# Optimization experiments

Hardware: AMD Instinct MI355X
Metric: run time of the kernel (lower is better)

The kernel has to match this reference:

```python
import jax, jax.numpy as jnp
import numpy as np

B, NM, D, H = 16384, 5, 256, 8
LN_EPS = 1e-5


def _ln(x, g, b):
    m = jnp.mean(x, axis=-1, keepdims=True)
    v = jnp.var(x, axis=-1, keepdims=True)
    return (x - m) / jnp.sqrt(v + LN_EPS) * g + b


def _mha(q_in, kv_in, Wi, bi, Wo, bo):
    # q_in: [B,1,D], kv_in: [B,1,D]; Wi: [3D,D] packed q/k/v like nn.MultiheadAttention
    Bq, Lq, Dm = q_in.shape
    Lk = kv_in.shape[1]
    dh = Dm // H
    q = (q_in @ Wi[:Dm].T + bi[:Dm]).reshape(Bq, Lq, H, dh).transpose(0, 2, 1, 3)
    k = (kv_in @ Wi[Dm:2 * Dm].T + bi[Dm:2 * Dm]).reshape(Bq, Lk, H, dh).transpose(0, 2, 1, 3)
    v = (kv_in @ Wi[2 * Dm:].T + bi[2 * Dm:]).reshape(Bq, Lk, H, dh).transpose(0, 2, 1, 3)
    scores = jnp.einsum('bhqd,bhkd->bhqk', q, k) * (1.0 / np.sqrt(dh))
    attn = jax.nn.softmax(scores, axis=-1)  # trivially 1.0 for Lk=1, kept for fidelity
    out = jnp.einsum('bhqk,bhkd->bhqd', attn, v).transpose(0, 2, 1, 3).reshape(Bq, Lq, Dm)
    return out @ Wo.T + bo


def setup_inputs() -> dict:
    key = jax.random.key(0)
    ks = jax.random.split(key, 8)
    s = 0.02
    return {
        'x': jax.random.normal(ks[0], (B, NM, D), jnp.float32),
        'self_Wi': jax.random.normal(ks[1], (3 * D, D), jnp.float32) * s,
        'self_bi': jnp.zeros((3 * D,), jnp.float32),
        'self_Wo': jax.random.normal(ks[2], (D, D), jnp.float32) * s,
        'self_bo': jnp.zeros((D,), jnp.float32),
        'cross_Wi': jax.random.normal(ks[3], (4, 3 * D, D), jnp.float32) * s,
        'cross_bi': jnp.zeros((4, 3 * D), jnp.float32),
        'cross_Wo': jax.random.normal(ks[4], (4, D, D), jnp.float32) * s,
        'cross_bo': jnp.zeros((4, D), jnp.float32),
        'cross_ln_g': jnp.ones((4, D), jnp.float32),
        'cross_ln_b': jnp.zeros((4, D), jnp.float32),
        'gate_ln_g': jnp.ones((D,), jnp.float32),
        'gate_ln_b': jnp.zeros((D,), jnp.float32),
        'gate_W': jax.random.normal(ks[5], (NM, D), jnp.float32) * s,
        'gate_b': jnp.zeros((NM,), jnp.float32),
        'final_ln_g': jnp.ones((D,), jnp.float32),
        'final_ln_b': jnp.zeros((D,), jnp.float32),
        'modal_idx': 2,
    }


def reference(x, self_Wi, self_bi, self_Wo, self_bo,
              cross_Wi, cross_bi, cross_Wo, cross_bo, cross_ln_g, cross_ln_b,
              gate_ln_g, gate_ln_b, gate_W, gate_b, final_ln_g, final_ln_b,
              modal_idx):
    query = x[:, modal_idx:modal_idx + 1, :]  # [B,1,D]
    self_out = _mha(query, query, self_Wi, self_bi, self_Wo, self_bo)

    other_idx = [i for i in range(NM) if i != modal_idx]
    kv = jnp.swapaxes(x[:, other_idx, :], 0, 1)[:, :, None, :]  # [4,B,1,D]

    def branch(Wi, bi, Wo, bo, g, b, kv_i):
        a = _mha(query, kv_i, Wi, bi, Wo, bo)
        return _ln(query + a, g, b)  # dropout is identity in eval

    cross_outs = jax.vmap(branch)(cross_Wi, cross_bi, cross_Wo, cross_bo,
                                  cross_ln_g, cross_ln_b, kv)  # [4,B,1,D]

    gates = jax.nn.softmax(_ln(query, gate_ln_g, gate_ln_b) @ gate_W.T + gate_b, axis=-1)  # [B,1,5]
    combined = gates[..., 0:1] * self_out + jnp.einsum('nbld,bln->bld', cross_outs, gates[..., 1:])
    return _ln(query + combined, final_ln_g, final_ln_b)
```

## Files before the change

kernel.cpp:

```cpp
#include <hip/hip_runtime.h>


typedef __attribute__((ext_vector_type(8))) short short8;
typedef __attribute__((ext_vector_type(4))) float floatx4;

__device__ __forceinline__ float b2f(unsigned short h) {
    union { unsigned int u; float f; } v; v.u = ((unsigned int)h) << 16; return v.f;
}
__device__ __forceinline__ unsigned short f2b(float f) {
    union { unsigned int u; float f; } v; v.f = f;
    unsigned int u = v.u;
    return (unsigned short)((u + 0x7FFFu + ((u >> 16) & 1u)) >> 16);
}

__global__ __launch_bounds__(256) void k_fuse(
    const float* __restrict__ sWi, const float* __restrict__ sbi,
    const float* __restrict__ sWo, const float* __restrict__ sbo,
    const float* __restrict__ cWi, const float* __restrict__ cbi,
    const float* __restrict__ cWo, const float* __restrict__ cbo,
    unsigned short* __restrict__ WF, float* __restrict__ BF)
{
    int s = blockIdx.y;
    int i0 = blockIdx.x * 4;
    int tid = threadIdx.x;
    const float *Wo, *Wv, *bv, *bo;
    if (s == 0) { Wo = sWo; Wv = sWi + 512 * 256; bv = sbi + 512; bo = sbo; }
    else {
        int n = s - 1;
        Wo = cWo + n * 65536;
        Wv = cWi + n * 768 * 256 + 512 * 256;
        bv = cbi + n * 768 + 512;
        bo = cbo + n * 256;
    }
    __shared__ float wo[4 * 256];
    #pragma unroll
    for (int it = 0; it < 4; ++it) {
        int idx = tid + it * 256;
        wo[idx] = Wo[i0 * 256 + idx];
    }
    __syncthreads();
    float a0 = 0.f, a1 = 0.f, a2 = 0.f, a3 = 0.f;
    for (int k = 0; k < 256; ++k) {
        float wv = Wv[k * 256 + tid];
        a0 += wo[k] * wv;
        a1 += wo[256 + k] * wv;
        a2 += wo[512 + k] * wv;
        a3 += wo[768 + k] * wv;
    }
    unsigned short* dst = WF + ((size_t)s * 256 + i0) * 256 + tid;
    dst[0] = f2b(a0); dst[256] = f2b(a1); dst[512] = f2b(a2); dst[768] = f2b(a3);
    if (tid < 4) {
        int i = i0 + tid;
        float bacc = 0.f;
        for (int k = 0; k < 256; ++k) bacc += Wo[i * 256 + k] * bv[k];
        BF[s * 256 + i] = bacc + bo[i];
    }
}

__device__ __forceinline__ float wred(float v) {
    #pragma unroll
    for (int o = 32; o > 0; o >>= 1) v += __shfl_xor(v, o, 64);
    return v;
}

__global__ __launch_bounds__(256) void k_main(
    const float* __restrict__ x, const unsigned short* __restrict__ WF,
    const float* __restrict__ BF,
    const float* __restrict__ cln_g, const float* __restrict__ cln_b,
    const float* __restrict__ gln_g, const float* __restrict__ gln_b,
    const float* __restrict__ gW, const float* __restrict__ gb,
    const float* __restrict__ fln_g, const float* __restrict__ fln_b,
    const int* __restrict__ midx, float* __restrict__ out)
{
    __shared__ __align__(16) unsigned short A[32 * 264];
    __shared__ __align__(16) unsigned short Yb[32 * 264];
    __shared__ float gWs[5 * 256];
    __shared__ float gLDS[32 * 8];

    int m = midx[0];
    int b0 = blockIdx.x * 32;
    int tid = threadIdx.x;
    int wave = tid >> 6, lane = tid & 63;
    int l16 = lane & 15, q4 = lane >> 4;
    int j = lane * 4;

    #pragma unroll
    for (int i = 0; i < 5; ++i) gWs[tid + i * 256] = gW[tid + i * 256];

    float qv[8][4];
    #pragma unroll
    for (int rr = 0; rr < 8; ++rr) {
        int r = wave * 8 + rr;
        float4 u = *(const float4*)(x + ((size_t)(b0 + r) * 5 + m) * 256 + j);
        qv[rr][0] = u.x; qv[rr][1] = u.y; qv[rr][2] = u.z; qv[rr][3] = u.w;
    }
    float4 glg = *(const float4*)(gln_g + j);
    float4 glb = *(const float4*)(gln_b + j);
    float gbv[5];
    #pragma unroll
    for (int n = 0; n < 5; ++n) gbv[n] = gb[n];

    __syncthreads();

    #pragma unroll
    for (int rr = 0; rr < 8; ++rr) {
        int r = wave * 8 + rr;
        float s1 = wred(qv[rr][0] + qv[rr][1] + qv[rr][2] + qv[rr][3]);
        float s2 = wred(qv[rr][0]*qv[rr][0] + qv[rr][1]*qv[rr][1] +
                        qv[rr][2]*qv[rr][2] + qv[rr][3]*qv[rr][3]);
        float mn = s1 * (1.f / 256.f);
        float vr = s2 * (1.f / 256.f) - mn * mn;
        float rs = rsqrtf(vr + 1e-5f);
        float qln[4];
        qln[0] = (qv[rr][0] - mn) * rs * glg.x + glb.x;
        qln[1] = (qv[rr][1] - mn) * rs * glg.y + glb.y;
        qln[2] = (qv[rr][2] - mn) * rs * glg.z + glb.z;
        qln[3] = (qv[rr][3] - mn) * rs * glg.w + glb.w;
        float g[5];
        #pragma unroll
        for (int n = 0; n < 5; ++n) {
            float p = qln[0] * gWs[n * 256 + j] + qln[1] * gWs[n * 256 + j + 1]
                    + qln[2] * gWs[n * 256 + j + 2] + qln[3] * gWs[n * 256 + j + 3];
            g[n] = wred(p) + gbv[n];
        }
        float mx = g[0];
        #pragma unroll
        for (int n = 1; n < 5; ++n) mx = fmaxf(mx, g[n]);
        float es = 0.f;
        #pragma unroll
        for (int n = 0; n < 5; ++n) { g[n] = __expf(g[n] - mx); es += g[n]; }
        float inv = 1.f / es;
        if (lane == 0) {
            #pragma unroll
            for (int n = 0; n < 5; ++n) gLDS[r * 8 + n] = g[n] * inv;
        }
    }

    float comb[8][4];
    #pragma unroll
    for (int rr = 0; rr < 8; ++rr)
        #pragma unroll
        for (int i = 0; i < 4; ++i) comb[rr][i] = 0.f;

    for (int s = 0; s < 5; ++s) {
        int mod = (s == 0) ? m : ((s - 1 < m) ? s - 1 : s);
        #pragma unroll
        for (int it = 0; it < 8; ++it) {
            int c = tid + it * 256;
            int row = c >> 6;
            int c4 = (c & 63) << 2;
            float4 v = *(const float4*)(x + ((size_t)(b0 + row) * 5 + mod) * 256 + c4);
            uint2 p;
            p.x = (unsigned int)f2b(v.x) | ((unsigned int)f2b(v.y) << 16);
            p.y = (unsigned int)f2b(v.z) | ((unsigned int)f2b(v.w) << 16);
            *(uint2*)(&A[row * 264 + c4]) = p;
        }
        __syncthreads();

        floatx4 acc[2][4];
        #pragma unroll
        for (int rt = 0; rt < 2; ++rt)
            #pragma unroll
            for (int ct = 0; ct < 4; ++ct) acc[rt][ct] = (floatx4){0.f, 0.f, 0.f, 0.f};
        const unsigned short* wB = WF + (size_t)s * 65536;
        #pragma unroll
        for (int kk = 0; kk < 8; ++kk) {
            int k = kk * 32 + q4 * 8;
            short8 a0 = *(const short8*)(&A[l16 * 264 + k]);
            short8 a1 = *(const short8*)(&A[(16 + l16) * 264 + k]);
            short8 bb[4];
            #pragma unroll
            for (int ct = 0; ct < 4; ++ct)
                bb[ct] = *(const short8*)(wB + (size_t)(wave * 64 + ct * 16 + l16) * 256 + k);
            #pragma unroll
            for (int ct = 0; ct < 4; ++ct) {
                acc[0][ct] = __builtin_amdgcn_mfma_f32_16x16x32_bf16(a0, bb[ct], acc[0][ct], 0, 0, 0);
                acc[1][ct] = __builtin_amdgcn_mfma_f32_16x16x32_bf16(a1, bb[ct], acc[1][ct], 0, 0, 0);
            }
        }
        #pragma unroll
        for (int rt = 0; rt < 2; ++rt)
            #pragma unroll
            for (int i = 0; i < 4; ++i) {
                int r = rt * 16 + q4 * 4 + i;
                #pragma unroll
                for (int ct = 0; ct < 4; ++ct)
                    Yb[r * 264 + wave * 64 + ct * 16 + l16] = f2b(acc[rt][ct][i]);
            }
        __syncthreads();

        float4 bfv = *(const float4*)(BF + s * 256 + j);
        if (s == 0) {
            #pragma unroll
            for (int rr = 0; rr < 8; ++rr) {
                int r = wave * 8 + rr;
                uint2 u = *(const uint2*)(&Yb[r * 264 + j]);
                float y0 = b2f(u.x & 0xffff) + bfv.x, y1 = b2f(u.x >> 16) + bfv.y;
                float y2 = b2f(u.y & 0xffff) + bfv.z, y3 = b2f(u.y >> 16) + bfv.w;
                float g0 = gLDS[r * 8 + 0];
                comb[rr][0] += g0 * y0; comb[rr][1] += g0 * y1;
                comb[rr][2] += g0 * y2; comb[rr][3] += g0 * y3;
            }
        } else {
            float4 cg = *(const float4*)(cln_g + (s - 1) * 256 + j);
            float4 cb = *(const float4*)(cln_b + (s - 1) * 256 + j);
            #pragma unroll
            for (int rr = 0; rr < 8; ++rr) {
                int r = wave * 8 + rr;
                uint2 u = *(const uint2*)(&Yb[r * 264 + j]);
                float t0 = qv[rr][0] + b2f(u.x & 0xffff) + bfv.x;
                float t1 = qv[rr][1] + b2f(u.x >> 16)    + bfv.y;
                float t2 = qv[rr][2] + b2f(u.y & 0xffff) + bfv.z;
                float t3 = qv[rr][3] + b2f(u.y >> 16)    + bfv.w;
                float s1 = wred(t0 + t1 + t2 + t3);
                float s2 = wred(t0*t0 + t1*t1 + t2*t2 + t3*t3);
                float mn = s1 * (1.f / 256.f);
                float vr = s2 * (1.f / 256.f) - mn * mn;
                float rs = rsqrtf(vr + 1e-5f);
                float gs = gLDS[r * 8 + s];
                comb[rr][0] += gs * ((t0 - mn) * rs * cg.x + cb.x);
                comb[rr][1] += gs * ((t1 - mn) * rs * cg.y + cb.y);
                comb[rr][2] += gs * ((t2 - mn) * rs * cg.z + cb.z);
                comb[rr][3] += gs * ((t3 - mn) * rs * cg.w + cb.w);
            }
        }
    }

    float4 fg = *(const float4*)(fln_g + j);
    float4 fb = *(const float4*)(fln_b + j);
    #pragma unroll
    for (int rr = 0; rr < 8; ++rr) {
        int r = wave * 8 + rr;
        float t0 = qv[rr][0] + comb[rr][0], t1 = qv[rr][1] + comb[rr][1];
        float t2 = qv[rr][2] + comb[rr][2], t3 = qv[rr][3] + comb[rr][3];
        float s1 = wred(t0 + t1 + t2 + t3);
        float s2 = wred(t0*t0 + t1*t1 + t2*t2 + t3*t3);
        float mn = s1 * (1.f / 256.f);
        float vr = s2 * (1.f / 256.f) - mn * mn;
        float rs = rsqrtf(vr + 1e-5f);
        float4 ov;
        ov.x = (t0 - mn) * rs * fg.x + fb.x;
        ov.y = (t1 - mn) * rs * fg.y + fb.y;
        ov.z = (t2 - mn) * rs * fg.z + fb.z;
        ov.w = (t3 - mn) * rs * fg.w + fb.w;
        *(float4*)(out + (size_t)(b0 + r) * 256 + j) = ov;
    }
}

extern "C" void kernel_launch(void* const* d_in, const int* in_sizes, int n_in,
                              void* d_out, int out_size, void* d_ws, size_t ws_size,
                              hipStream_t stream) {
    const float* x    = (const float*)d_in[0];
    const float* sWi  = (const float*)d_in[1];
    const float* sbi  = (const float*)d_in[2];
    const float* sWo  = (const float*)d_in[3];
    const float* sbo  = (const float*)d_in[4];
    const float* cWi  = (const float*)d_in[5];
    const float* cbi  = (const float*)d_in[6];
    const float* cWo  = (const float*)d_in[7];
    const float* cbo  = (const float*)d_in[8];
    const float* clng = (const float*)d_in[9];
    const float* clnb = (const float*)d_in[10];
    const float* glng = (const float*)d_in[11];
    const float* glnb = (const float*)d_in[12];
    const float* gW   = (const float*)d_in[13];
    const float* gb   = (const float*)d_in[14];
    const float* flng = (const float*)d_in[15];
    const float* flnb = (const float*)d_in[16];
    const int* midx   = (const int*)d_in[17];
    float* out        = (float*)d_out;

    char* ws = (char*)d_ws;
    unsigned short* WF = (unsigned short*)ws;
    float* BF          = (float*)(ws + 655360);

    k_fuse<<<dim3(64, 5), 256, 0, stream>>>(sWi, sbi, sWo, sbo, cWi, cbi, cWo, cbo, WF, BF);
    k_main<<<512, 256, 0, stream>>>(x, WF, BF, clng, clnb, glng, glnb, gW, gb, flng, flnb, midx, out);
}
```

Measured before the change: 227.0 us.

## Stage all modalities once per block, halve rows per block, use DPP reductions

```diff
diff --git a/kernel.cpp b/kernel.cpp
--- a/kernel.cpp
+++ b/kernel.cpp
@@ -4,13 +4,25 @@
 typedef __attribute__((ext_vector_type(8))) short short8;
 typedef __attribute__((ext_vector_type(4))) float floatx4;
 
-__device__ __forceinline__ float b2f(unsigned short h) {
-    union { unsigned int u; float f; } v; v.u = ((unsigned int)h) << 16; return v.f;
-}
-__device__ __forceinline__ unsigned short f2b(float f) {
-    union { unsigned int u; float f; } v; v.f = f;
-    unsigned int u = v.u;
+__device__ __forceinline__ float b2f(unsigned short h){ return __uint_as_float((unsigned)h << 16); }
+__device__ __forceinline__ unsigned short f2b(float f){
+    unsigned u = __float_as_uint(f);
     return (unsigned short)((u + 0x7FFFu + ((u >> 16) & 1u)) >> 16);
+}
+
+template<int CTRL>
+__device__ __forceinline__ float dpp_add(float v){
+    int x = __builtin_amdgcn_update_dpp(0, __float_as_int(v), CTRL, 0xf, 0xf, true);
+    return v + __int_as_float(x);
+}
+__device__ __forceinline__ float wsum(float v){
+    v = dpp_add<0x111>(v);
+    v = dpp_add<0x112>(v);
+    v = dpp_add<0x114>(v);
+    v = dpp_add<0x118>(v);
+    v = dpp_add<0x142>(v);
+    v = dpp_add<0x143>(v);
+    return __int_as_float(__builtin_amdgcn_readlane(__float_as_int(v), 63));
 }
 
 __global__ __launch_bounds__(256) void k_fuse(
@@ -23,6 +35,7 @@
     int s = blockIdx.y;
     int i0 = blockIdx.x * 4;
     int tid = threadIdx.x;
+    int wave = tid >> 6, lane = tid & 63;
     const float *Wo, *Wv, *bv, *bo;
     if (s == 0) { Wo = sWo; Wv = sWi + 512 * 256; bv = sbi + 512; bo = sbo; }
     else {
@@ -40,6 +53,7 @@
     }
     __syncthreads();
     float a0 = 0.f, a1 = 0.f, a2 = 0.f, a3 = 0.f;
+    #pragma unroll 8
     for (int k = 0; k < 256; ++k) {
         float wv = Wv[k * 256 + tid];
         a0 += wo[k] * wv;
@@ -49,21 +63,17 @@
     }
     unsigned short* dst = WF + ((size_t)s * 256 + i0) * 256 + tid;
     dst[0] = f2b(a0); dst[256] = f2b(a1); dst[512] = f2b(a2); dst[768] = f2b(a3);
-    if (tid < 4) {
-        int i = i0 + tid;
-        float bacc = 0.f;
-        for (int k = 0; k < 256; ++k) bacc += Wo[i * 256 + k] * bv[k];
-        BF[s * 256 + i] = bacc + bo[i];
-    }
-}
-
-__device__ __forceinline__ float wred(float v) {
-    #pragma unroll
-    for (int o = 32; o > 0; o >>= 1) v += __shfl_xor(v, o, 64);
-    return v;
-}
-
-__global__ __launch_bounds__(256) void k_main(
+    {
+        int i = i0 + wave;
+        float4 a = *(const float4*)(Wo + (size_t)i * 256 + lane * 4);
+        float4 b = *(const float4*)(bv + lane * 4);
+        float p = a.x * b.x + a.y * b.y + a.z * b.z + a.w * b.w;
+        p = wsum(p);
+        if (lane == 0) BF[s * 256 + i] = p + bo[i];
+    }
+}
+
+__global__ __launch_bounds__(256, 3) void k_main(
     const float* __restrict__ x, const unsigned short* __restrict__ WF,
     const float* __restrict__ BF,
     const float* __restrict__ cln_g, const float* __restrict__ cln_b,
@@ -72,169 +82,157 @@
     const float* __restrict__ fln_g, const float* __restrict__ fln_b,
     const int* __restrict__ midx, float* __restrict__ out)
 {
-    __shared__ __align__(16) unsigned short A[32 * 264];
-    __shared__ __align__(16) unsigned short Yb[32 * 264];
-    __shared__ float gWs[5 * 256];
-    __shared__ float gLDS[32 * 8];
+    __shared__ __align__(16) unsigned short Ax[20480];
+    __shared__ __align__(16) unsigned short Yb[16 * 264];
 
     int m = midx[0];
-    int b0 = blockIdx.x * 32;
+    int b0 = blockIdx.x * 16;
     int tid = threadIdx.x;
     int wave = tid >> 6, lane = tid & 63;
     int l16 = lane & 15, q4 = lane >> 4;
-    int j = lane * 4;
-
-    #pragma unroll
-    for (int i = 0; i < 5; ++i) gWs[tid + i * 256] = gW[tid + i * 256];
-
-    float qv[8][4];
-    #pragma unroll
-    for (int rr = 0; rr < 8; ++rr) {
-        int r = wave * 8 + rr;
-        float4 u = *(const float4*)(x + ((size_t)(b0 + r) * 5 + m) * 256 + j);
-        qv[rr][0] = u.x; qv[rr][1] = u.y; qv[rr][2] = u.z; qv[rr][3] = u.w;
-    }
-    float4 glg = *(const float4*)(gln_g + j);
-    float4 glb = *(const float4*)(gln_b + j);
+
+    #pragma unroll
+    for (int it = 0; it < 20; ++it) {
+        int idx = tid + it * 256;
+        int row = idx / 320;
+        int rem = idx - row * 320;
+        int mod = rem >> 6;
+        int c = (rem & 63) << 2;
+        float4 v = *(const float4*)(x + (size_t)b0 * 1280 + (size_t)idx * 4);
+        int kk = c >> 5, qq = (c >> 3) & 3, j = c & 7;
+        int slot = row ^ ((kk * 4 + qq) & 15);
+        uint2 p;
+        p.x = (unsigned)f2b(v.x) | ((unsigned)f2b(v.y) << 16);
+        p.y = (unsigned)f2b(v.z) | ((unsigned)f2b(v.w) << 16);
+        *(uint2*)(Ax + ((((mod * 8 + kk) * 4 + qq) * 16 + slot) * 8 + j)) = p;
+    }
+
+    float4 qv[4];
+    #pragma unroll
+    for (int rr = 0; rr < 4; ++rr)
+        qv[rr] = *(const float4*)(x + ((size_t)(b0 + wave * 4 + rr) * 5 + m) * 256 + lane * 4);
+
+    __syncthreads();
+
+    float4 glg = *(const float4*)(gln_g + lane * 4);
+    float4 glb = *(const float4*)(gln_b + lane * 4);
+    float4 gwv[5];
     float gbv[5];
     #pragma unroll
-    for (int n = 0; n < 5; ++n) gbv[n] = gb[n];
-
-    __syncthreads();
-
-    #pragma unroll
-    for (int rr = 0; rr < 8; ++rr) {
-        int r = wave * 8 + rr;
-        float s1 = wred(qv[rr][0] + qv[rr][1] + qv[rr][2] + qv[rr][3]);
-        float s2 = wred(qv[rr][0]*qv[rr][0] + qv[rr][1]*qv[rr][1] +
-                        qv[rr][2]*qv[rr][2] + qv[rr][3]*qv[rr][3]);
+    for (int n = 0; n < 5; ++n) {
+        gwv[n] = *(const float4*)(gW + n * 256 + lane * 4);
+        gbv[n] = gb[n];
+    }
+    float gte[4][5];
+    #pragma unroll
+    for (int rr = 0; rr < 4; ++rr) {
+        float s1 = wsum(qv[rr].x + qv[rr].y + qv[rr].z + qv[rr].w);
+        float s2 = wsum(qv[rr].x * qv[rr].x + qv[rr].y * qv[rr].y +
+                        qv[rr].z * qv[rr].z + qv[rr].w * qv[rr].w);
         float mn = s1 * (1.f / 256.f);
         float vr = s2 * (1.f / 256.f) - mn * mn;
         float rs = rsqrtf(vr + 1e-5f);
-        float qln[4];
-        qln[0] = (qv[rr][0] - mn) * rs * glg.x + glb.x;
-        qln[1] = (qv[rr][1] - mn) * rs * glg.y + glb.y;
-        qln[2] = (qv[rr][2] - mn) * rs * glg.z + glb.z;
-        qln[3] = (qv[rr][3] - mn) * rs * glg.w + glb.w;
-        float g[5];
+        float q0 = (qv[rr].x - mn) * rs * glg.x + glb.x;
+        float q1 = (qv[rr].y - mn) * rs * glg.y + glb.y;
+        float q2 = (qv[rr].z - mn) * rs * glg.z + glb.z;
+        float q3 = (qv[rr].w - mn) * rs * glg.w + glb.w;
+        float lg[5];
         #pragma unroll
         for (int n = 0; n < 5; ++n) {
-            float p = qln[0] * gWs[n * 256 + j] + qln[1] * gWs[n * 256 + j + 1]
-                    + qln[2] * gWs[n * 256 + j + 2] + qln[3] * gWs[n * 256 + j + 3];
-            g[n] = wred(p) + gbv[n];
+            float p = q0 * gwv[n].x + q1 * gwv[n].y + q2 * gwv[n].z + q3 * gwv[n].w;
+            lg[n] = wsum(p) + gbv[n];
         }
-        float mx = g[0];
-        #pragma unroll
-        for (int n = 1; n < 5; ++n) mx = fmaxf(mx, g[n]);
+        float mx = lg[0];
+        #pragma unroll
+        for (int n = 1; n < 5; ++n) mx = fmaxf(mx, lg[n]);
         float es = 0.f;
         #pragma unroll
-        for (int n = 0; n < 5; ++n) { g[n] = __expf(g[n] - mx); es += g[n]; }
+        for (int n = 0; n < 5; ++n) { lg[n] = __expf(lg[n] - mx); es += lg[n]; }
         float inv = 1.f / es;
-        if (lane == 0) {
-            #pragma unroll
-            for (int n = 0; n < 5; ++n) gLDS[r * 8 + n] = g[n] * inv;
-        }
-    }
-
-    float comb[8][4];
-    #pragma unroll
-    for (int rr = 0; rr < 8; ++rr)
+        #pragma unroll
+        for (int n = 0; n < 5; ++n) gte[rr][n] = lg[n] * inv;
+    }
+
+    float comb[4][4];
+    #pragma unroll
+    for (int rr = 0; rr < 4; ++rr)
         #pragma unroll
         for (int i = 0; i < 4; ++i) comb[rr][i] = 0.f;
 
     for (int s = 0; s < 5; ++s) {
         int mod = (s == 0) ? m : ((s - 1 < m) ? s - 1 : s);
-        #pragma unroll
-        for (int it = 0; it < 8; ++it) {
-            int c = tid + it * 256;
-            int row = c >> 6;
-            int c4 = (c & 63) << 2;
-            float4 v = *(const float4*)(x + ((size_t)(b0 + row) * 5 + mod) * 256 + c4);
-            uint2 p;
-            p.x = (unsigned int)f2b(v.x) | ((unsigned int)f2b(v.y) << 16);
-            p.y = (unsigned int)f2b(v.z) | ((unsigned int)f2b(v.w) << 16);
-            *(uint2*)(&A[row * 264 + c4]) = p;
+        floatx4 acc[4];
+        #pragma unroll
+        for (int ct = 0; ct < 4; ++ct) acc[ct] = (floatx4){0.f, 0.f, 0.f, 0.f};
+        const unsigned short* wB = WF + (size_t)s * 65536;
+        #pragma unroll
+        for (int kk = 0; kk < 8; ++kk) {
+            int slot = l16 ^ ((kk * 4 + q4) & 15);
+            short8 a = *(const short8*)(Ax + (((mod * 8 + kk) * 4 + q4) * 16 + slot) * 8);
+            short8 bb[4];
+            #pragma unroll
+            for (int ct = 0; ct < 4; ++ct)
+                bb[ct] = *(const short8*)(wB + (size_t)(wave * 64 + ct * 16 + l16) * 256 + kk * 32 + q4 * 8);
+            #pragma unroll
+            for (int ct = 0; ct < 4; ++ct)
+                acc[ct] = __builtin_amdgcn_mfma_f32_16x16x32_bf16(a, bb[ct], acc[ct], 0, 0, 0);
         }
+        #pragma unroll
+        for (int ct = 0; ct < 4; ++ct)
+            #pragma unroll
+            for (int i = 0; i < 4; ++i)
+                Yb[(q4 * 4 + i) * 264 + wave * 64 + ct * 16 + l16] = f2b(acc[ct][i]);
         __syncthreads();
 
-        floatx4 acc[2][4];
-        #pragma unroll
-        for (int rt = 0; rt < 2; ++rt)
-            #pragma unroll
-            for (int ct = 0; ct < 4; ++ct) acc[rt][ct] = (floatx4){0.f, 0.f, 0.f, 0.f};
-        const unsigned short* wB = WF + (size_t)s * 65536;
-        #pragma unroll
-        for (int kk = 0; kk < 8; ++kk) {
-            int k = kk * 32 + q4 * 8;
-            short8 a0 = *(const short8*)(&A[l16 * 264 + k]);
-            short8 a1 = *(const short8*)(&A[(16 + l16) * 264 + k]);
-            short8 bb[4];
-            #pragma unroll
-            for (int ct = 0; ct < 4; ++ct)
-                bb[ct] = *(const short8*)(wB + (size_t)(wave * 64 + ct * 16 + l16) * 256 + k);
-            #pragma unroll
-            for (int ct = 0; ct < 4; ++ct) {
-                acc[0][ct] = __builtin_amdgcn_mfma_f32_16x16x32_bf16(a0, bb[ct], acc[0][ct], 0, 0, 0);
-                acc[1][ct] = __builtin_amdgcn_mfma_f32_16x16x32_bf16(a1, bb[ct], acc[1][ct], 0, 0, 0);
-            }
-        }
-        #pragma unroll
-        for (int rt = 0; rt < 2; ++rt)
-            #pragma unroll
-            for (int i = 0; i < 4; ++i) {
-                int r = rt * 16 + q4 * 4 + i;
-                #pragma unroll
-                for (int ct = 0; ct < 4; ++ct)
-                    Yb[r * 264 + wave * 64 + ct * 16 + l16] = f2b(acc[rt][ct][i]);
-            }
-        __syncthreads();
-
-        float4 bfv = *(const float4*)(BF + s * 256 + j);
+        float4 bfv = *(const float4*)(BF + s * 256 + lane * 4);
         if (s == 0) {
             #pragma unroll
-            for (int rr = 0; rr < 8; ++rr) {
-                int r = wave * 8 + rr;
-                uint2 u = *(const uint2*)(&Yb[r * 264 + j]);
-                float y0 = b2f(u.x & 0xffff) + bfv.x, y1 = b2f(u.x >> 16) + bfv.y;
-                float y2 = b2f(u.y & 0xffff) + bfv.z, y3 = b2f(u.y >> 16) + bfv.w;
-                float g0 = gLDS[r * 8 + 0];
-                comb[rr][0] += g0 * y0; comb[rr][1] += g0 * y1;
-                comb[rr][2] += g0 * y2; comb[rr][3] += g0 * y3;
+            for (int rr = 0; rr < 4; ++rr) {
+                int row = wave * 4 + rr;
+                uint2 u = *(const uint2*)(Yb + row * 264 + lane * 4);
+                float g0 = gte[rr][0];
+                comb[rr][0] += g0 * (b2f(u.x & 0xffff) + bfv.x);
+                comb[rr][1] += g0 * (b2f(u.x >> 16) + bfv.y);
+                comb[rr][2] += g0 * (b2f(u.y & 0xffff) + bfv.z);
+                comb[rr][3] += g0 * (b2f(u.y >> 16) + bfv.w);
             }
         } else {
-            float4 cg = *(const float4*)(cln_g + (s - 1) * 256 + j);
-            float4 cb = *(const float4*)(cln_b + (s - 1) * 256 + j);
-            #pragma unroll
-            for (int rr = 0; rr < 8; ++rr) {
-                int r = wave * 8 + rr;
-                uint2 u = *(const uint2*)(&Yb[r * 264 + j]);
-                float t0 = qv[rr][0] + b2f(u.x & 0xffff) + bfv.x;
-                float t1 = qv[rr][1] + b2f(u.x >> 16)    + bfv.y;
-                float t2 = qv[rr][2] + b2f(u.y & 0xffff) + bfv.z;
-                float t3 = qv[rr][3] + b2f(u.y >> 16)    + bfv.w;
-                float s1 = wred(t0 + t1 + t2 + t3);
-                float s2 = wred(t0*t0 + t1*t1 + t2*t2 + t3*t3);
+            float4 cg = *(const float4*)(cln_g + (s - 1) * 256 + lane * 4);
+            float4 cb = *(const float4*)(cln_b + (s - 1) * 256 + lane * 4);
+            #pragma unroll
+            for (int rr = 0; rr < 4; ++rr) {
+                int row = wave * 4 + rr;
+                uint2 u = *(const uint2*)(Yb + row * 264 + lane * 4);
+                float t0 = qv[rr].x + b2f(u.x & 0xffff) + bfv.x;
+                float t1 = qv[rr].y + b2f(u.x >> 16) + bfv.y;
+                float t2 = qv[rr].z + b2f(u.y & 0xffff) + bfv.z;
+                float t3 = qv[rr].w + b2f(u.y >> 16) + bfv.w;
+                float s1 = wsum(t0 + t1 + t2 + t3);
+                float s2 = wsum(t0 * t0 + t1 * t1 + t2 * t2 + t3 * t3);
                 float mn = s1 * (1.f / 256.f);
                 float vr = s2 * (1.f / 256.f) - mn * mn;
                 float rs = rsqrtf(vr + 1e-5f);
-                float gs = gLDS[r * 8 + s];
+                float gs = gte[rr][s];
                 comb[rr][0] += gs * ((t0 - mn) * rs * cg.x + cb.x);
                 comb[rr][1] += gs * ((t1 - mn) * rs * cg.y + cb.y);
                 comb[rr][2] += gs * ((t2 - mn) * rs * cg.z + cb.z);
                 comb[rr][3] += gs * ((t3 - mn) * rs * cg.w + cb.w);
             }
         }
-    }
-
-    float4 fg = *(const float4*)(fln_g + j);
-    float4 fb = *(const float4*)(fln_b + j);
-    #pragma unroll
-    for (int rr = 0; rr < 8; ++rr) {
-        int r = wave * 8 + rr;
-        float t0 = qv[rr][0] + comb[rr][0], t1 = qv[rr][1] + comb[rr][1];
-        float t2 = qv[rr][2] + comb[rr][2], t3 = qv[rr][3] + comb[rr][3];
-        float s1 = wred(t0 + t1 + t2 + t3);
-        float s2 = wred(t0*t0 + t1*t1 + t2*t2 + t3*t3);
+        __syncthreads();
+    }
+
+    float4 fg = *(const float4*)(fln_g + lane * 4);
+    float4 fb = *(const float4*)(fln_b + lane * 4);
+    #pragma unroll
+    for (int rr = 0; rr < 4; ++rr) {
+        int row = wave * 4 + rr;
+        float t0 = qv[rr].x + comb[rr][0];
+        float t1 = qv[rr].y + comb[rr][1];
+        float t2 = qv[rr].z + comb[rr][2];
+        float t3 = qv[rr].w + comb[rr][3];
+        float s1 = wsum(t0 + t1 + t2 + t3);
+        float s2 = wsum(t0 * t0 + t1 * t1 + t2 * t2 + t3 * t3);
         float mn = s1 * (1.f / 256.f);
         float vr = s2 * (1.f / 256.f) - mn * mn;
         float rs = rsqrtf(vr + 1e-5f);
@@ -243,7 +241,7 @@
         ov.y = (t1 - mn) * rs * fg.y + fb.y;
         ov.z = (t2 - mn) * rs * fg.z + fb.z;
         ov.w = (t3 - mn) * rs * fg.w + fb.w;
-        *(float4*)(out + (size_t)(b0 + r) * 256 + j) = ov;
+        *(float4*)(out + (size_t)(b0 + row) * 256 + lane * 4) = ov;
     }
 }
 
@@ -275,5 +273,5 @@
     float* BF          = (float*)(ws + 655360);
 
     k_fuse<<<dim3(64, 5), 256, 0, stream>>>(sWi, sbi, sWo, sbo, cWi, cbi, cWo, cbo, WF, BF);
-    k_main<<<512, 256, 0, stream>>>(x, WF, BF, clng, clnb, glng, glnb, gW, gb, flng, flnb, midx, out);
-}
+    k_main<<<1024, 256, 0, stream>>>(x, WF, BF, clng, clnb, glng, glnb, gW, gb, flng, flnb, midx, out);
+}
```

Measured after the change: 272.5 us. 20.1% more time.
